# Performance work log

Hardware: AMD Instinct MI355X
Metric: run time of the kernel (lower is better)

## Reference

```python
import jax, jax.numpy as jnp
import numpy as np

N = 50000
E = 1000000


def _edge_sage(x, edge_attr, src, dst, Wn, bn, Ws, bs):
    # message: lin_neigh(concat(x_j, edge_attr)); x_j = x[src] (PyG source_to_target)
    msg = jnp.concatenate([x[src], edge_attr], axis=-1) @ Wn + bn  # [E+N, out]
    agg = jax.ops.segment_sum(msg, dst, num_segments=x.shape[0])
    cnt = jax.ops.segment_sum(jnp.ones((dst.shape[0],), msg.dtype), dst,
                              num_segments=x.shape[0])
    mean = agg / cnt[:, None]  # self-loops guarantee cnt >= 1
    return jax.nn.relu(x @ Ws + bs + mean)


def setup_inputs() -> dict:
    key = jax.random.key(0)
    ks = jax.random.split(key, 12)
    din, dedge, dh, dout = 64, 16, 64, 64
    s = lambda f: 1.0 / np.sqrt(f)
    return {
        "x": jax.random.normal(ks[0], (N, din), jnp.float32),
        "edge_index": jax.random.randint(ks[1], (2, E), 0, N, jnp.int32),
        "edge_attr": jax.random.normal(ks[2], (E, dedge), jnp.float32),
        "W1n": jax.random.uniform(ks[3], (din + dedge, dh), jnp.float32, -s(din + dedge), s(din + dedge)),
        "b1n": jax.random.uniform(ks[4], (dh,), jnp.float32, -s(din + dedge), s(din + dedge)),
        "W1s": jax.random.uniform(ks[5], (din, dh), jnp.float32, -s(din), s(din)),
        "b1s": jax.random.uniform(ks[6], (dh,), jnp.float32, -s(din), s(din)),
        "W2n": jax.random.uniform(ks[7], (dh + dedge, dout), jnp.float32, -s(dh + dedge), s(dh + dedge)),
        "b2n": jax.random.uniform(ks[8], (dout,), jnp.float32, -s(dh + dedge), s(dh + dedge)),
        "W2s": jax.random.uniform(ks[9], (dh, dout), jnp.float32, -s(dh), s(dh)),
        "b2s": jax.random.uniform(ks[10], (dout,), jnp.float32, -s(dh), s(dh)),
    }


def reference(x, edge_index, edge_attr, W1n, b1n, W1s, b1s, W2n, b2n, W2s, b2s):
    n = x.shape[0]
    loops = jnp.arange(n, dtype=edge_index.dtype)
    src = jnp.concatenate([edge_index[0], loops])
    dst = jnp.concatenate([edge_index[1], loops])
    ea = jnp.concatenate(
        [edge_attr, jnp.zeros((n, edge_attr.shape[1]), edge_attr.dtype)], axis=0)
    h = _edge_sage(x, ea, src, dst, W1n, b1n, W1s, b1s)
    return _edge_sage(h, ea, src, dst, W2n, b2n, W2s, b2s)
```

## Files before the change

### kernel.cpp

```cpp
#include <hip/hip_runtime.h>

#define N_NODES 50000
#define NE 1000000
#define NBLK 196
#define NBUK 196
#define CHUNK 4096

typedef float vfloat4 __attribute__((ext_vector_type(4)));
typedef unsigned short ushort4v __attribute__((ext_vector_type(4)));
typedef unsigned short ushort8v __attribute__((ext_vector_type(8)));

__device__ __forceinline__ unsigned short f2b(float f) {
  unsigned u = __float_as_uint(f);
  u += 0x7FFF + ((u >> 16) & 1);
  return (unsigned short)(u >> 16);
}
__device__ __forceinline__ float b2f(unsigned short h) {
  return __uint_as_float(((unsigned)h) << 16);
}


__global__ __launch_bounds__(256) void hist_kernel(
    const int* __restrict__ ei, int* __restrict__ HIST) {
  int e = blockIdx.x * 256 + threadIdx.x;
  if (e >= NE) return;
  atomicAdd(&HIST[ei[NE + e]], 1);
}

__global__ __launch_bounds__(256) void scan_local(
    const int* __restrict__ HIST, int* __restrict__ OFF, int* __restrict__ BSUM) {
  __shared__ int s[256];
  int t = threadIdx.x;
  int g = blockIdx.x * 256 + t;
  int v = (g < N_NODES) ? HIST[g] : 0;
  s[t] = v;
  __syncthreads();
  #pragma unroll
  for (int off = 1; off < 256; off <<= 1) {
    int u = (t >= off) ? s[t - off] : 0;
    __syncthreads();
    s[t] += u;
    __syncthreads();
  }
  if (t == 255) BSUM[blockIdx.x] = s[255];
  if (g < N_NODES) OFF[g] = s[t] - v;
}

__global__ __launch_bounds__(256) void scan_bsums(
    int* __restrict__ BSUM, int* __restrict__ OFF) {
  __shared__ int s[256];
  int t = threadIdx.x;
  int v = (t < NBLK) ? BSUM[t] : 0;
  s[t] = v;
  __syncthreads();
  #pragma unroll
  for (int off = 1; off < 256; off <<= 1) {
    int u = (t >= off) ? s[t - off] : 0;
    __syncthreads();
    s[t] += u;
    __syncthreads();
  }
  if (t < NBLK) BSUM[t] = s[t] - v;
  if (t == 255) OFF[N_NODES] = s[255];
}

__global__ __launch_bounds__(256) void scan_add(
    int* __restrict__ OFF, const int* __restrict__ BSUM) {
  int g = blockIdx.x * 256 + threadIdx.x;
  if (g >= N_NODES) return;
  OFF[g] += BSUM[blockIdx.x];
}

__global__ __launch_bounds__(256) void init_bcur(
    const int* __restrict__ OFF, int* __restrict__ BCUR) {
  int b = threadIdx.x;
  BCUR[b] = OFF[min(b << 8, N_NODES)];
}

__global__ __launch_bounds__(256) void bucket_scatter(
    const int* __restrict__ ei, int* __restrict__ BCUR,
    long long* __restrict__ BKT) {
  __shared__ int cnt[256], sscan[256], base[256], cur[256], gb[256];
  __shared__ long long binned[CHUNK];
  __shared__ unsigned short dstl[CHUNK];
  int t = threadIdx.x;
  int c0 = blockIdx.x * CHUNK;
  int n = min(CHUNK, NE - c0);
  cnt[t] = 0;
  __syncthreads();
  for (int i = t; i < n; i += 256) {
    int dst = ei[NE + c0 + i];
    atomicAdd(&cnt[dst >> 8], 1);
  }
  __syncthreads();
  int myc = cnt[t];
  sscan[t] = myc;
  __syncthreads();
  #pragma unroll
  for (int off = 1; off < 256; off <<= 1) {
    int u = (t >= off) ? sscan[t - off] : 0;
    __syncthreads();
    sscan[t] += u;
    __syncthreads();
  }
  base[t] = sscan[t] - myc;
  cur[t] = sscan[t] - myc;
  if (myc > 0) gb[t] = atomicAdd(&BCUR[t], myc);
  __syncthreads();
  for (int i = t; i < n; i += 256) {
    int src = ei[c0 + i];
    int dst = ei[NE + c0 + i];
    int b = dst >> 8;
    int lp = atomicAdd(&cur[b], 1);
    binned[lp] = ((long long)(c0 + i) << 25) | ((long long)src << 8)
               | (long long)(dst & 255);
    dstl[lp] = (unsigned short)dst;
  }
  __syncthreads();
  for (int i = t; i < n; i += 256) {
    int b = ((int)dstl[i]) >> 8;
    BKT[gb[b] + (i - base[b])] = binned[i];
  }
}

__global__ __launch_bounds__(1024) void bucket_sort(
    const long long* __restrict__ BKT, const int* __restrict__ OFF,
    long long* __restrict__ SRT) {
  __shared__ int lcur[256];
  int t = threadIdx.x;
  if (t < 256) lcur[t] = 0;
  __syncthreads();
  int b = blockIdx.x;
  int nb0 = b << 8;
  int nb1 = min(nb0 + 256, N_NODES);
  int s0 = OFF[nb0], s1 = OFF[nb1];
  for (int p = s0 + t; p < s1; p += 1024) {
    long long pl = BKT[p];
    int dl = (int)(pl & 255);
    int idx = atomicAdd(&lcur[dl], 1);
    SRT[OFF[nb0 + dl] + idx] = pl;
  }
}

__global__ __launch_bounds__(256) void conv_bf16(
    const float* __restrict__ in, unsigned short* __restrict__ out) {
  int i = blockIdx.x * 256 + threadIdx.x;
  if (i >= (N_NODES * 64) / 4) return;
  vfloat4 v = ((const vfloat4*)in)[i];
  ushort4v o = { f2b(v[0]), f2b(v[1]), f2b(v[2]), f2b(v[3]) };
  ((ushort4v*)out)[i] = o;
}

template <bool HAS_EA>
__global__ __launch_bounds__(256) void gather_agg(
    const unsigned short* __restrict__ XB,
    const float* __restrict__ ea,
    const long long* __restrict__ SRT, const int* __restrict__ OFF,
    float* __restrict__ AGG,
    float* __restrict__ AEout)
{
  int w = (blockIdx.x * 256 + threadIdx.x) >> 6;
  int lane = threadIdx.x & 63;
  if (w >= N_NODES) return;
  int s0 = OFF[w], s1 = OFF[w + 1];
  int slot = lane >> 3;
  int j = lane & 7;
  float ax[8] = {0.f,0.f,0.f,0.f,0.f,0.f,0.f,0.f};
  float ae0=0.f, ae1=0.f, ae2=0.f, ae3=0.f;
  for (int p = s0 + slot; p < s1; p += 8) {
    long long pl = SRT[p];
    int src = (int)((pl >> 8) & 0x1FFFF);
    ushort8v v = ((const ushort8v*)XB)[src * 8 + j];
    #pragma unroll
    for (int k = 0; k < 8; ++k) ax[k] += b2f(v[k]);
    if (HAS_EA) {
      int eid = (int)(pl >> 25);
      if (j < 4) {
        vfloat4 ev = *(const vfloat4*)(ea + eid * 16 + j * 4);
        ae0 += ev[0]; ae1 += ev[1]; ae2 += ev[2]; ae3 += ev[3];
      }
    }
  }
  #pragma unroll
  for (int m = 8; m <= 32; m <<= 1) {
    #pragma unroll
    for (int k = 0; k < 8; ++k) ax[k] += __shfl_xor(ax[k], m, 64);
    if (HAS_EA) {
      ae0 += __shfl_xor(ae0, m, 64);
      ae1 += __shfl_xor(ae1, m, 64);
      ae2 += __shfl_xor(ae2, m, 64);
      ae3 += __shfl_xor(ae3, m, 64);
    }
  }
  if (lane < 8) {
    vfloat4 o0 = {ax[0], ax[1], ax[2], ax[3]};
    vfloat4 o1 = {ax[4], ax[5], ax[6], ax[7]};
    *(vfloat4*)(AGG + w * 64 + lane * 8) = o0;
    *(vfloat4*)(AGG + w * 64 + lane * 8 + 4) = o1;
  }
  if (HAS_EA && lane < 4) {
    vfloat4 oe = {ae0, ae1, ae2, ae3};
    *(vfloat4*)(AEout + w * 16 + lane * 4) = oe;
  }
}

template <bool XBF, bool OBF>
__global__ __launch_bounds__(256) void layer_kernel(
    const void* __restrict__ xin_, const float* __restrict__ AGG,
    const float* __restrict__ AE, const int* __restrict__ OFF,
    const float* __restrict__ Ws, const float* __restrict__ bs,
    const float* __restrict__ Wn, const float* __restrict__ bn,
    void* __restrict__ out_)
{
  __shared__ float Ml[144][68];
  __shared__ float Wl[72][64];
  __shared__ float biasl[64];
  __shared__ float invl[64];

  const float* xf = (const float*)xin_;
  const unsigned short* xb = (const unsigned short*)xin_;

  int t = threadIdx.x;
  int base = blockIdx.x * 64;

  if (t < 64) {
    int i = base + t;
    float deg = (i < N_NODES) ? (float)(OFF[i + 1] - OFF[i]) : 0.0f;
    invl[t] = 1.0f / (deg + 1.0f);
    biasl[t] = bs[t] + bn[t];
  }
  __syncthreads();

  for (int idx = t; idx < 4096; idx += 256) {
    int r = idx >> 6, k = idx & 63;
    int i = base + r;
    float xv = 0.f, av = 0.f;
    if (i < N_NODES) {
      xv = XBF ? b2f(xb[i * 64 + k]) : xf[i * 64 + k];
      av = AGG[i * 64 + k];
    }
    Ml[k][r] = xv;
    Ml[64 + k][r] = (av + xv) * invl[r];
  }
  for (int idx = t; idx < 1024; idx += 256) {
    int r = idx >> 4, k = idx & 15;
    int i = base + r;
    Ml[128 + k][r] = (i < N_NODES) ? AE[i * 16 + k] * invl[r] : 0.0f;
  }

  int tx = t & 15;
  int ty = t >> 4;
  float acc[4][4] = {{0.f}};

  for (int kc = 0; kc < 2; ++kc) {
    for (int idx = t; idx < 72 * 64; idx += 256) {
      int lr = idx >> 6, c = idx & 63;
      int k = kc * 72 + lr;
      Wl[lr][c] = (k < 64) ? Ws[k * 64 + c] : Wn[(k - 64) * 64 + c];
    }
    __syncthreads();
    #pragma unroll 8
    for (int k = 0; k < 72; ++k) {
      float4 a = *(const float4*)&Ml[kc * 72 + k][ty * 4];
      float4 b = *(const float4*)&Wl[k][tx * 4];
      float av[4] = {a.x, a.y, a.z, a.w};
      float bv[4] = {b.x, b.y, b.z, b.w};
      #pragma unroll
      for (int ri = 0; ri < 4; ++ri)
        #pragma unroll
        for (int ci = 0; ci < 4; ++ci)
          acc[ri][ci] = fmaf(av[ri], bv[ci], acc[ri][ci]);
    }
    __syncthreads();
  }

  #pragma unroll
  for (int ri = 0; ri < 4; ++ri) {
    int i = base + ty * 4 + ri;
    if (i < N_NODES) {
      float o0 = fmaxf(acc[ri][0] + biasl[tx * 4 + 0], 0.0f);
      float o1 = fmaxf(acc[ri][1] + biasl[tx * 4 + 1], 0.0f);
      float o2 = fmaxf(acc[ri][2] + biasl[tx * 4 + 2], 0.0f);
      float o3 = fmaxf(acc[ri][3] + biasl[tx * 4 + 3], 0.0f);
      if (OBF) {
        ushort4v ob = { f2b(o0), f2b(o1), f2b(o2), f2b(o3) };
        ((ushort4v*)out_)[i * 16 + tx] = ob;
      } else {
        float4 of = {o0, o1, o2, o3};
        ((float4*)out_)[i * 16 + tx] = of;
      }
    }
  }
}

extern "C" void kernel_launch(void* const* d_in, const int* in_sizes, int n_in,
                              void* d_out, int out_size, void* d_ws, size_t ws_size,
                              hipStream_t stream) {
  const float* x   = (const float*)d_in[0];
  const int*   ei  = (const int*)d_in[1];
  const float* ea  = (const float*)d_in[2];
  const float* W1n = (const float*)d_in[3];
  const float* b1n = (const float*)d_in[4];
  const float* W1s = (const float*)d_in[5];
  const float* b1s = (const float*)d_in[6];
  const float* W2n = (const float*)d_in[7];
  const float* b2n = (const float*)d_in[8];
  const float* W2s = (const float*)d_in[9];
  const float* b2s = (const float*)d_in[10];

  int* wsi = (int*)d_ws;
  float* wsf = (float*)d_ws;
  int*  OFF  = wsi;
  long long* SRT = (long long*)(wsi + 50004);
  unsigned short* XB = (unsigned short*)(wsi + 2050004);
  float* AE  = wsf + 3650004;
  int*  BCUR = wsi + 4450004;
  long long* BKT = (long long*)(wsi + 4450260);
  int*  HIST = wsi + 4450260;
  int*  BSUM = wsi + 4500260;
  float* AGG = (float*)d_out;
  float* out = (float*)d_out;

  hipMemsetAsync(HIST, 0, N_NODES * 4, stream);

  hist_kernel<<<(NE + 255) / 256, 256, 0, stream>>>(ei, HIST);
  scan_local<<<NBLK, 256, 0, stream>>>(HIST, OFF, BSUM);
  scan_bsums<<<1, 256, 0, stream>>>(BSUM, OFF);
  scan_add<<<NBLK, 256, 0, stream>>>(OFF, BSUM);
  init_bcur<<<1, 256, 0, stream>>>(OFF, BCUR);
  bucket_scatter<<<(NE + CHUNK - 1) / CHUNK, 256, 0, stream>>>(ei, BCUR, BKT);
  bucket_sort<<<NBUK, 1024, 0, stream>>>(BKT, OFF, SRT);
  conv_bf16<<<(N_NODES * 64 / 4 + 255) / 256, 256, 0, stream>>>(x, XB);

  gather_agg<true><<<12500, 256, 0, stream>>>(XB, ea, SRT, OFF, AGG, AE);
  layer_kernel<false, true><<<782, 256, 0, stream>>>(
      x, AGG, AE, OFF, W1s, b1s, W1n, b1n, XB);
  gather_agg<false><<<12500, 256, 0, stream>>>(XB, nullptr, SRT, OFF, AGG, nullptr);
  layer_kernel<true, false><<<782, 256, 0, stream>>>(
      XB, AGG, AE, OFF, W2s, b2s, W2n, b2n, out);
}
```

Before: 237.9 us.

## Replace per-node histogram and multi-pass scan with bucket-level counts and in-block sort offsets

Drops the global per-node histogram with its million atomics and the three-kernel scan. Edges are now counted per 256-node bucket using shared-memory atomics, and a single small scan produces the bucket offsets. bucket_sort stages each bucket in LDS, builds its own per-node histogram and scan, and writes the CSR offsets itself. Nontemporal loads and stores are added on the streaming buffers. The cost is a large LDS buffer in bucket_sort, with a fallback to global reads when a bucket exceeds its capacity.

```diff
diff --git a/kernel.cpp b/kernel.cpp
--- a/kernel.cpp
+++ b/kernel.cpp
@@ -2,9 +2,9 @@
 
 #define N_NODES 50000
 #define NE 1000000
-#define NBLK 196
 #define NBUK 196
 #define CHUNK 4096
+#define MAXBE 6144
 
 typedef float vfloat4 __attribute__((ext_vector_type(4)));
 typedef unsigned short ushort4v __attribute__((ext_vector_type(4)));
@@ -20,19 +20,27 @@
 }
 
 
-__global__ __launch_bounds__(256) void hist_kernel(
-    const int* __restrict__ ei, int* __restrict__ HIST) {
-  int e = blockIdx.x * 256 + threadIdx.x;
-  if (e >= NE) return;
-  atomicAdd(&HIST[ei[NE + e]], 1);
-}
-
-__global__ __launch_bounds__(256) void scan_local(
-    const int* __restrict__ HIST, int* __restrict__ OFF, int* __restrict__ BSUM) {
+
+__global__ __launch_bounds__(256) void bucket_count(
+    const int* __restrict__ ei, int* __restrict__ BCNT) {
+  __shared__ int c[256];
+  int t = threadIdx.x;
+  c[t] = 0;
+  __syncthreads();
+  int i0 = blockIdx.x * CHUNK;
+  int n = min(CHUNK, NE - i0);
+  for (int i = t; i < n; i += 256)
+    atomicAdd(&c[ei[NE + i0 + i] >> 8], 1);
+  __syncthreads();
+  if (t < NBUK && c[t] > 0) atomicAdd(&BCNT[t], c[t]);
+}
+
+__global__ __launch_bounds__(256) void scan_buckets(
+    const int* __restrict__ BCNT, int* __restrict__ BOFF,
+    int* __restrict__ BCUR, int* __restrict__ OFF) {
   __shared__ int s[256];
   int t = threadIdx.x;
-  int g = blockIdx.x * 256 + t;
-  int v = (g < N_NODES) ? HIST[g] : 0;
+  int v = (t < NBUK) ? BCNT[t] : 0;
   s[t] = v;
   __syncthreads();
   #pragma unroll
@@ -42,39 +50,10 @@
     s[t] += u;
     __syncthreads();
   }
-  if (t == 255) BSUM[blockIdx.x] = s[255];
-  if (g < N_NODES) OFF[g] = s[t] - v;
-}
-
-__global__ __launch_bounds__(256) void scan_bsums(
-    int* __restrict__ BSUM, int* __restrict__ OFF) {
-  __shared__ int s[256];
-  int t = threadIdx.x;
-  int v = (t < NBLK) ? BSUM[t] : 0;
-  s[t] = v;
-  __syncthreads();
-  #pragma unroll
-  for (int off = 1; off < 256; off <<= 1) {
-    int u = (t >= off) ? s[t - off] : 0;
-    __syncthreads();
-    s[t] += u;
-    __syncthreads();
-  }
-  if (t < NBLK) BSUM[t] = s[t] - v;
-  if (t == 255) OFF[N_NODES] = s[255];
-}
-
-__global__ __launch_bounds__(256) void scan_add(
-    int* __restrict__ OFF, const int* __restrict__ BSUM) {
-  int g = blockIdx.x * 256 + threadIdx.x;
-  if (g >= N_NODES) return;
-  OFF[g] += BSUM[blockIdx.x];
-}
-
-__global__ __launch_bounds__(256) void init_bcur(
-    const int* __restrict__ OFF, int* __restrict__ BCUR) {
-  int b = threadIdx.x;
-  BCUR[b] = OFF[min(b << 8, N_NODES)];
+  int ex = s[t] - v;
+  if (t < NBUK) { BOFF[t] = ex; BCUR[t] = ex; }
+  if (t == NBUK - 1) BOFF[NBUK] = s[t];
+  if (t == 0) OFF[N_NODES] = NE;
 }
 
 __global__ __launch_bounds__(256) void bucket_scatter(
@@ -119,26 +98,46 @@
   __syncthreads();
   for (int i = t; i < n; i += 256) {
     int b = ((int)dstl[i]) >> 8;
-    BKT[gb[b] + (i - base[b])] = binned[i];
+    __builtin_nontemporal_store(binned[i], &BKT[gb[b] + (i - base[b])]);
   }
 }
 
 __global__ __launch_bounds__(1024) void bucket_sort(
-    const long long* __restrict__ BKT, const int* __restrict__ OFF,
-    long long* __restrict__ SRT) {
-  __shared__ int lcur[256];
-  int t = threadIdx.x;
-  if (t < 256) lcur[t] = 0;
+    const long long* __restrict__ BKT, const int* __restrict__ BOFF,
+    int* __restrict__ OFF, long long* __restrict__ SRT) {
+  __shared__ int cnt[256], ss[256], loff[256], cur[256];
+  __shared__ long long buf[MAXBE];
+  int t = threadIdx.x;
+  if (t < 256) { cnt[t] = 0; cur[t] = 0; }
   __syncthreads();
   int b = blockIdx.x;
+  int s0 = BOFF[b], s1 = BOFF[b + 1];
+  int n = s1 - s0;
+  for (int i = t; i < n; i += 1024) {
+    long long pl = __builtin_nontemporal_load(&BKT[s0 + i]);
+    if (i < MAXBE) buf[i] = pl;
+    atomicAdd(&cnt[(int)(pl & 255)], 1);
+  }
+  __syncthreads();
+  if (t < 256) ss[t] = cnt[t];
+  __syncthreads();
+  #pragma unroll
+  for (int off = 1; off < 256; off <<= 1) {
+    int u = 0;
+    if (t < 256 && t >= off) u = ss[t - off];
+    __syncthreads();
+    if (t < 256) ss[t] += u;
+    __syncthreads();
+  }
+  if (t < 256) loff[t] = ss[t] - cnt[t];
+  __syncthreads();
   int nb0 = b << 8;
-  int nb1 = min(nb0 + 256, N_NODES);
-  int s0 = OFF[nb0], s1 = OFF[nb1];
-  for (int p = s0 + t; p < s1; p += 1024) {
-    long long pl = BKT[p];
+  if (t < 256 && nb0 + t < N_NODES) OFF[nb0 + t] = s0 + loff[t];
+  for (int i = t; i < n; i += 1024) {
+    long long pl = (i < MAXBE) ? buf[i] : __builtin_nontemporal_load(&BKT[s0 + i]);
     int dl = (int)(pl & 255);
-    int idx = atomicAdd(&lcur[dl], 1);
-    SRT[OFF[nb0 + dl] + idx] = pl;
+    int p = atomicAdd(&cur[dl], 1);
+    SRT[s0 + loff[dl] + p] = pl;
   }
 }
 
@@ -168,7 +167,7 @@
   float ax[8] = {0.f,0.f,0.f,0.f,0.f,0.f,0.f,0.f};
   float ae0=0.f, ae1=0.f, ae2=0.f, ae3=0.f;
   for (int p = s0 + slot; p < s1; p += 8) {
-    long long pl = SRT[p];
+    long long pl = __builtin_nontemporal_load(&SRT[p]);
     int src = (int)((pl >> 8) & 0x1FFFF);
     ushort8v v = ((const ushort8v*)XB)[src * 8 + j];
     #pragma unroll
@@ -176,7 +175,7 @@
     if (HAS_EA) {
       int eid = (int)(pl >> 25);
       if (j < 4) {
-        vfloat4 ev = *(const vfloat4*)(ea + eid * 16 + j * 4);
+        vfloat4 ev = __builtin_nontemporal_load((const vfloat4*)(ea + eid * 16 + j * 4));
         ae0 += ev[0]; ae1 += ev[1]; ae2 += ev[2]; ae3 += ev[3];
       }
     }
@@ -195,12 +194,12 @@
   if (lane < 8) {
     vfloat4 o0 = {ax[0], ax[1], ax[2], ax[3]};
     vfloat4 o1 = {ax[4], ax[5], ax[6], ax[7]};
-    *(vfloat4*)(AGG + w * 64 + lane * 8) = o0;
-    *(vfloat4*)(AGG + w * 64 + lane * 8 + 4) = o1;
+    __builtin_nontemporal_store(o0, (vfloat4*)(AGG + w * 64 + lane * 8));
+    __builtin_nontemporal_store(o1, (vfloat4*)(AGG + w * 64 + lane * 8 + 4));
   }
   if (HAS_EA && lane < 4) {
     vfloat4 oe = {ae0, ae1, ae2, ae3};
-    *(vfloat4*)(AEout + w * 16 + lane * 4) = oe;
+    __builtin_nontemporal_store(oe, (vfloat4*)(AEout + w * 16 + lane * 4));
   }
 }
 
@@ -314,22 +313,20 @@
   long long* SRT = (long long*)(wsi + 50004);
   unsigned short* XB = (unsigned short*)(wsi + 2050004);
   float* AE  = wsf + 3650004;
-  int*  BCUR = wsi + 4450004;
-  long long* BKT = (long long*)(wsi + 4450260);
-  int*  HIST = wsi + 4450260;
-  int*  BSUM = wsi + 4500260;
+  int*  BCNT = wsi + 4450004;
+  int*  BOFF = wsi + 4450260;
+  int*  BCUR = wsi + 4450516;
+  long long* BKT = (long long*)(wsi + 4450772);
   float* AGG = (float*)d_out;
   float* out = (float*)d_out;
 
-  hipMemsetAsync(HIST, 0, N_NODES * 4, stream);
-
-  hist_kernel<<<(NE + 255) / 256, 256, 0, stream>>>(ei, HIST);
-  scan_local<<<NBLK, 256, 0, stream>>>(HIST, OFF, BSUM);
-  scan_bsums<<<1, 256, 0, stream>>>(BSUM, OFF);
-  scan_add<<<NBLK, 256, 0, stream>>>(OFF, BSUM);
-  init_bcur<<<1, 256, 0, stream>>>(OFF, BCUR);
-  bucket_scatter<<<(NE + CHUNK - 1) / CHUNK, 256, 0, stream>>>(ei, BCUR, BKT);
-  bucket_sort<<<NBUK, 1024, 0, stream>>>(BKT, OFF, SRT);
+  hipMemsetAsync(BCNT, 0, 256 * 4, stream);
+
+  int cb = (NE + CHUNK - 1) / CHUNK;
+  bucket_count<<<cb, 256, 0, stream>>>(ei, BCNT);
+  scan_buckets<<<1, 256, 0, stream>>>(BCNT, BOFF, BCUR, OFF);
+  bucket_scatter<<<cb, 256, 0, stream>>>(ei, BCUR, BKT);
+  bucket_sort<<<NBUK, 1024, 0, stream>>>(BKT, BOFF, OFF, SRT);
   conv_bf16<<<(N_NODES * 64 / 4 + 255) / 256, 256, 0, stream>>>(x, XB);
 
   gather_agg<true><<<12500, 256, 0, stream>>>(XB, ea, SRT, OFF, AGG, AE);
```

Result: faster. 217.0 us (-8.8%).
